# Kernel tuning notes

Measured on AMD Instinct MI355X. Metric: run time of the kernel, lower is better.

Reference implementation:

```python
import jax, jax.numpy as jnp
import numpy as np

B, Q, N, C = 2, 1024, 4096, 768
H, D, REL = 12, 64, 32
SCALE = 1.0 / np.sqrt(D)


def _lin_coords(n_out, n_in):
    # align_corners=True mapping: x_in = x_out * (n_in-1)/(n_out-1)
    pos = jnp.arange(n_out, dtype=jnp.float32) * ((n_in - 1) / (n_out - 1))
    lo = jnp.clip(jnp.floor(pos).astype(jnp.int32), 0, n_in - 1)
    hi = jnp.clip(lo + 1, 0, n_in - 1)
    w = pos - lo.astype(jnp.float32)
    return lo, hi, w


def _interp_bias(bias, q_len, n_len):
    # bias: [H, 32, 32] -> [H, q_len, n_len] bilinear, align_corners=True
    lq, hq, wq = _lin_coords(q_len, REL)
    ln, hn, wn = _lin_coords(n_len, REL)
    b1 = bias[:, lq, :] * (1.0 - wq)[None, :, None] + bias[:, hq, :] * wq[None, :, None]  # [H,q,32]
    b2 = b1[:, :, ln] * (1.0 - wn)[None, None, :] + b1[:, :, hn] * wn[None, None, :]      # [H,q,n]
    return b2


def setup_inputs() -> dict:
    key = jax.random.key(0)
    ks = jax.random.split(key, 11)
    s = 1.0 / np.sqrt(C)
    return {
        "query": jax.random.normal(ks[0], (B, Q, C), jnp.float32),
        "key_value": jax.random.normal(ks[1], (B, N, C), jnp.float32),
        "Wq": jax.random.normal(ks[2], (C, C), jnp.float32) * s,
        "bq": jax.random.normal(ks[3], (C,), jnp.float32) * 0.01,
        "Wk": jax.random.normal(ks[4], (C, C), jnp.float32) * s,
        "bk": jax.random.normal(ks[5], (C,), jnp.float32) * 0.01,
        "Wv": jax.random.normal(ks[6], (C, C), jnp.float32) * s,
        "bv": jax.random.normal(ks[7], (C,), jnp.float32) * 0.01,
        "Wo": jax.random.normal(ks[8], (C, C), jnp.float32) * s,
        "bo": jax.random.normal(ks[9], (C,), jnp.float32) * 0.01,
        "rel_pos_bias": jax.random.normal(ks[10], (H, REL, REL), jnp.float32) * 0.02,
    }


def reference(query, key_value, Wq, bq, Wk, bk, Wv, bv, Wo, bo, rel_pos_bias):
    b, n, c = key_value.shape
    q_len = query.shape[1]
    # projections (dropout in eval mode -> identity)
    q = (query @ Wq + bq).reshape(b, q_len, H, D).transpose(0, 2, 1, 3)      # [B,H,Q,D]
    k = (key_value @ Wk + bk).reshape(b, n, H, D).transpose(0, 2, 1, 3)      # [B,H,N,D]
    v = (key_value @ Wv + bv).reshape(b, n, H, D).transpose(0, 2, 1, 3)      # [B,H,N,D]
    attn = jnp.einsum('bhqd,bhnd->bhqn', q, k) * SCALE
    attn = attn + _interp_bias(rel_pos_bias, q_len, n)[None]                 # [B,H,Q,N]
    p = jax.nn.softmax(attn, axis=-1)
    out = jnp.einsum('bhqn,bhnd->bhqd', p, v)
    out = out.transpose(0, 2, 1, 3).reshape(b, q_len, c)
    return out @ Wo + bo
```

## Files before the change

### kernel.cpp

```cpp
#include <hip/hip_runtime.h>
#include <stdint.h>

typedef unsigned short ushort_t;
typedef __bf16 bf16x8 __attribute__((ext_vector_type(8)));
typedef __bf16 bf16x4v __attribute__((ext_vector_type(4)));
typedef float f32x4 __attribute__((ext_vector_type(4)));
typedef unsigned short us4 __attribute__((ext_vector_type(4)));

#define LOG2E 1.4426950408889634f
#define NEG8L (-11.541560327111707f)
#define QSCALE 0.18033688011110974f

__device__ __forceinline__ ushort_t f2b(float f) {
    unsigned u = __float_as_uint(f);
    unsigned r = (u + 0x7fffu + ((u >> 16) & 1u)) >> 16;
    return (ushort_t)r;
}
__device__ __forceinline__ void gld16(const void* g, void* l) {
    __builtin_amdgcn_global_load_lds(
        (__attribute__((address_space(1))) void*)g,
        (__attribute__((address_space(3))) void*)l,
        16, 0, 0);
}

__global__ __launch_bounds__(256) void prep(
        const float* __restrict__ query, const float* __restrict__ keyv,
        const float* __restrict__ Wq, const float* __restrict__ Wk,
        const float* __restrict__ Wv, const float* __restrict__ Wo,
        const float* __restrict__ rel,
        ushort_t* __restrict__ qc, ushort_t* __restrict__ kvc,
        ushort_t* __restrict__ wtq, ushort_t* __restrict__ wtk,
        ushort_t* __restrict__ wtv, ushort_t* __restrict__ wto,
        ushort_t* __restrict__ b1b, ushort_t* __restrict__ wtab) {
    __shared__ ushort_t tsh[32][33];
    const int bid = blockIdx.x, tid = threadIdx.x;
    if (bid < 7680) {
        const float* src = (bid < 1536) ? query : keyv;
        ushort_t* dst = (bid < 1536) ? qc : kvc;
        int i = ((bid < 1536) ? bid : bid - 1536) * 256 + tid;
        float4 x = ((const float4*)src)[i];
        us4 v; v.x = f2b(x.x); v.y = f2b(x.y); v.z = f2b(x.z); v.w = f2b(x.w);
        ((us4*)dst)[i] = v;
    } else if (bid < 9984) {
        int t = bid - 7680, w = t / 576, tt = t - w * 576;
        const float* in = (w == 0) ? Wq : (w == 1) ? Wk : (w == 2) ? Wv : Wo;
        ushort_t* out = (w == 0) ? wtq : (w == 1) ? wtk : (w == 2) ? wtv : wto;
        int x = tid & 31, y = tid >> 5;
        int bx = (tt % 24) * 32, by = (tt / 24) * 32;
#pragma unroll
        for (int j = 0; j < 32; j += 8)
            tsh[y + j][x] = f2b(in[(size_t)(by + y + j) * 768 + bx + x]);
        __syncthreads();
#pragma unroll
        for (int j = 0; j < 32; j += 8)
            out[(size_t)(bx + y + j) * 768 + by + x] = tsh[x][y + j];
    } else if (bid < 11520) {
        int idx = (bid - 9984) * 256 + tid;
        int j = idx & 31, q = (idx >> 5) & 1023, h = idx >> 15;
        float pos = q * (31.0f / 1023.0f);
        float fl = floorf(pos);
        int lo = (int)fl; if (lo > 31) lo = 31;
        float w = pos - fl;
        int hi = lo + 1; if (hi > 31) hi = 31;
        float vlo = rel[(h * 32 + lo) * 32 + j];
        float vhi = rel[(h * 32 + hi) * 32 + j];
        b1b[idx] = f2b((vlo + (vhi - vlo) * w) * LOG2E);
    } else {
        int n = (bid - 11520) * 256 + tid;
        float pos = n * (31.0f / 4095.0f);
        float fl = floorf(pos);
        int ln = (int)fl; if (ln > 31) ln = 31;
        float wn = pos - fl;
        int hn = ln + 1; if (hn > 31) hn = 31;
        float vals[32];
#pragma unroll
        for (int j = 0; j < 32; ++j) vals[j] = 0.f;
        vals[ln] += 1.0f - wn;
        vals[hn] += wn;
#pragma unroll
        for (int j = 0; j < 32; ++j) wtab[n * 32 + j] = f2b(vals[j]);
    }
}

__device__ __forceinline__ void gemm_store(const float* __restrict__ bias,
                                           f32x4 a, void* out,
                                           int mode, int lsh, float scale,
                                           int mbase, int n) {
    if (mode == 2) {
        int h = n >> 6, d = n & 63;
        int b = mbase >> lsh, l = mbase & ((1 << lsh) - 1);
        float bvf = bias[n];
        us4 v;
        v.x = f2b((a[0] + bvf) * scale);
        v.y = f2b((a[1] + bvf) * scale);
        v.z = f2b((a[2] + bvf) * scale);
        v.w = f2b((a[3] + bvf) * scale);
        *(us4*)((ushort_t*)out + ((size_t)((b * 12 + h) * 64 + d) << lsh) + l) = v;
    } else if (mode == 3) {
        int h = mbase >> 6, dbase = mbase & 63;
        int b = n >> lsh, l = n & ((1 << lsh) - 1);
        us4 v;
        v.x = f2b((a[0] + bias[mbase + 0]) * scale);
        v.y = f2b((a[1] + bias[mbase + 1]) * scale);
        v.z = f2b((a[2] + bias[mbase + 2]) * scale);
        v.w = f2b((a[3] + bias[mbase + 3]) * scale);
        *(us4*)((ushort_t*)out + ((((size_t)(b * 12 + h) << lsh) + l) << 6) + dbase) = v;
    } else {
        float4 v;
        v.x = (a[0] + bias[mbase + 0]) * scale;
        v.y = (a[1] + bias[mbase + 1]) * scale;
        v.z = (a[2] + bias[mbase + 2]) * scale;
        v.w = (a[3] + bias[mbase + 3]) * scale;
        *(float4*)((float*)out + (size_t)n * 768 + mbase) = v;
    }
}

__device__ __forceinline__ void gemm_body128(const ushort_t* __restrict__ A,
                                             const ushort_t* __restrict__ Bt,
                                             const float* __restrict__ bias,
                                             void* __restrict__ out,
                                             int mode, int lsh, float scale,
                                             int m0, int n0,
                                             ushort_t* As, ushort_t* Bs, int tid) {
    const int wave = tid >> 6, lane = tid & 63;
    const int quad = lane >> 4, l15 = lane & 15;
    const int wm = wave >> 1, wn = wave & 1;
    const f32x4 z4 = {0.f, 0.f, 0.f, 0.f};
    f32x4 acc[4][4];
#pragma unroll
    for (int i = 0; i < 4; ++i)
#pragma unroll
        for (int j = 0; j < 4; ++j) acc[i][j] = z4;

    const int arow4 = lane >> 4;
    const int ablk16 = lane & 15;

    for (int kk = 0; kk < 768; kk += 128) {
        __syncthreads();
#pragma unroll
        for (int i = 0; i < 8; ++i) {
            int c = wave * 8 + i;
            int row = c * 4 + arow4;
            int swz = (ablk16 ^ (row & 15)) * 8;
            gld16(A + (size_t)(m0 + row) * 768 + kk + swz, (void*)(As + c * 512));
            gld16(Bt + (size_t)(n0 + row) * 768 + kk + swz, (void*)(Bs + c * 512));
        }
        __syncthreads();
#pragma unroll
        for (int ks = 0; ks < 4; ++ks) {
            bf16x8 af[4], bf[4];
#pragma unroll
            for (int mb = 0; mb < 4; ++mb) {
                int r = wm * 64 + mb * 16 + l15;
                af[mb] = *(const bf16x8*)(As + r * 128 + (((ks * 4 + quad) ^ (r & 15)) * 8));
            }
#pragma unroll
            for (int nb = 0; nb < 4; ++nb) {
                int r = wn * 64 + nb * 16 + l15;
                bf[nb] = *(const bf16x8*)(Bs + r * 128 + (((ks * 4 + quad) ^ (r & 15)) * 8));
            }
#pragma unroll
            for (int mb = 0; mb < 4; ++mb)
#pragma unroll
                for (int nb = 0; nb < 4; ++nb)
                    acc[mb][nb] = __builtin_amdgcn_mfma_f32_16x16x32_bf16(af[mb], bf[nb], acc[mb][nb], 0, 0, 0);
        }
    }

#pragma unroll
    for (int mb = 0; mb < 4; ++mb) {
        int mbase = m0 + wm * 64 + mb * 16 + quad * 4;
#pragma unroll
        for (int nb = 0; nb < 4; ++nb) {
            int n = n0 + wn * 64 + nb * 16 + l15;
            gemm_store(bias, acc[mb][nb], out, mode, lsh, scale, mbase, n);
        }
    }
}

__device__ __forceinline__ void gemm_body64(const ushort_t* __restrict__ A,
                                            const ushort_t* __restrict__ Bt,
                                            const float* __restrict__ bias,
                                            void* __restrict__ out,
                                            int mode, int lsh, float scale,
                                            int m0, int n0,
                                            ushort_t* As, ushort_t* Bs, int tid) {
    const int wave = tid >> 6, lane = tid & 63;
    const int quad = lane >> 4, l15 = lane & 15;
    const f32x4 z4 = {0.f, 0.f, 0.f, 0.f};
    f32x4 acc[4];
#pragma unroll
    for (int j = 0; j < 4; ++j) acc[j] = z4;

    const int arow = lane >> 3;
    const int ablk = lane & 7;
    const int kswz = (ablk ^ arow) * 8;

    for (int kk = 0; kk < 768; kk += 64) {
        __syncthreads();
#pragma unroll
        for (int i = 0; i < 2; ++i) {
            int c = wave * 2 + i;
            gld16(A + (size_t)(m0 + c * 8 + arow) * 768 + kk + kswz, (void*)(As + c * 512));
            gld16(Bt + (size_t)(n0 + c * 8 + arow) * 768 + kk + kswz, (void*)(Bs + c * 512));
        }
        __syncthreads();
#pragma unroll
        for (int ks = 0; ks < 2; ++ks) {
            bf16x8 af, bf[4];
            {
                int r = wave * 16 + l15;
                af = *(const bf16x8*)(As + r * 64 + (((ks * 4 + quad) ^ (r & 7)) * 8));
            }
#pragma unroll
            for (int nb = 0; nb < 4; ++nb) {
                int r = nb * 16 + l15;
                bf[nb] = *(const bf16x8*)(Bs + r * 64 + (((ks * 4 + quad) ^ (r & 7)) * 8));
            }
#pragma unroll
            for (int nb = 0; nb < 4; ++nb)
                acc[nb] = __builtin_amdgcn_mfma_f32_16x16x32_bf16(af, bf[nb], acc[nb], 0, 0, 0);
        }
    }

    int mbase = m0 + wave * 16 + quad * 4;
#pragma unroll
    for (int nb = 0; nb < 4; ++nb) {
        int n = n0 + nb * 16 + l15;
        gemm_store(bias, acc[nb], out, mode, lsh, scale, mbase, n);
    }
}

__global__ __launch_bounds__(256) void proj3(const ushort_t* __restrict__ qc,
                                             const ushort_t* __restrict__ kvc,
                                             const ushort_t* __restrict__ wtq,
                                             const ushort_t* __restrict__ wtk,
                                             const ushort_t* __restrict__ wtv,
                                             const float* __restrict__ bq,
                                             const float* __restrict__ bk,
                                             const float* __restrict__ bv,
                                             ushort_t* __restrict__ qp,
                                             ushort_t* __restrict__ kp,
                                             ushort_t* __restrict__ vtp) {
    __shared__ __align__(16) ushort_t As[128 * 128];
    __shared__ __align__(16) ushort_t Bs[128 * 128];
    const int bid = blockIdx.x, tid = threadIdx.x;
    if (bid < 96) {
        int t = bid;
        int nt = (t & 7) + 8 * ((t >> 3) & 1), mt = t >> 4;
        gemm_body128(wtq, qc, bq, qp, 3, 10, QSCALE, mt * 128, nt * 128, As, Bs, tid);
    } else if (bid < 480) {
        int t = bid - 96;
        int nt = (t & 7) + 8 * ((t >> 3) & 7), mt = t >> 6;
        gemm_body128(wtk, kvc, bk, kp, 3, 12, 1.0f, mt * 128, nt * 128, As, Bs, tid);
    } else {
        int t = bid - 480, mt = t & 63, nt = t >> 6;
        gemm_body128(kvc, wtv, bv, vtp, 2, 12, 1.0f, mt * 128, nt * 128, As, Bs, tid);
    }
}

__global__ __launch_bounds__(256) void gemm_out(const ushort_t* __restrict__ ab,
                                                const ushort_t* __restrict__ wto,
                                                const float* __restrict__ bo,
                                                float* __restrict__ out) {
    __shared__ __align__(16) ushort_t As[64 * 64];
    __shared__ __align__(16) ushort_t Bs[64 * 64];
    const int bid = blockIdx.x, tid = threadIdx.x;
    int j = bid >> 3;
    int nt = (bid & 7) + 8 * (j & 3), mt = j >> 2;
    gemm_body64(wto, ab, bo, out, 4, 0, 1.0f, mt * 64, nt * 64, As, Bs, tid);
}

__global__ __launch_bounds__(256) void attn64s(const ushort_t* __restrict__ qp,
                                               const ushort_t* __restrict__ kp,
                                               const ushort_t* __restrict__ vt,
                                               const ushort_t* __restrict__ b1b,
                                               const ushort_t* __restrict__ wtab,
                                               float* __restrict__ po,
                                               float* __restrict__ pl) {
    __shared__ __align__(16) ushort_t k_s[128 * 64];
    __shared__ __align__(16) ushort_t v_s[64 * 128];
    __shared__ __align__(16) __bf16 pB[4][16 * 136];

    const int tid = threadIdx.x;
    const int wave = tid >> 6, lane = tid & 63;
    const int quad = lane >> 4, l15 = lane & 15;
    const int bid = blockIdx.x;
    const int xcd = bid & 7;
    const int slot = bid >> 3;
    const int g = xcd + 8 * (slot >> 5);
    const int member = slot & 31;
    const int b = g / 12, h = g - b * 12;
    const int qt = member & 15, sp = member >> 4;
    const int q0 = qt * 64;
    const int bh = g;

    const ushort_t* qg = qp + ((size_t)bh * 1024 + q0) * 64;
    const ushort_t* kg = kp + (size_t)bh * 4096 * 64;
    const ushort_t* vg = vt + (size_t)bh * 64 * 4096;

    const int rowq = wave * 16 + l15;
    bf16x8 aq[2];
#pragma unroll
    for (int ks = 0; ks < 2; ++ks)
        aq[ks] = *(const bf16x8*)(qg + (size_t)rowq * 64 + (ks * 4 + quad) * 8);
    bf16x8 ab1 = *(const bf16x8*)(b1b + ((size_t)(h * 1024 + q0 + rowq)) * 32 + quad * 8);

    const f32x4 mC = {NEG8L, NEG8L, NEG8L, NEG8L};
    const f32x4 z4 = {0.f, 0.f, 0.f, 0.f};
    f32x4 o[4];
    float lsum = 0.f;
#pragma unroll
    for (int d = 0; d < 4; ++d) o[d] = z4;

    const int arow = lane >> 3;
    const int ablk = lane & 7;
    const int arow4 = lane >> 4;
    const int ablk16 = lane & 15;
    const int nbase = sp * 2048;
    __bf16* pw = &pB[wave][0];

    for (int nt = 0; nt < 16; ++nt) {
        const int n0 = nbase + nt * 128;
        __syncthreads();
#pragma unroll
        for (int i = 0; i < 4; ++i) {
            int c = wave * 4 + i;
            int krow = c * 8 + arow;
            gld16(kg + (size_t)(n0 + krow) * 64 + (ablk ^ (krow & 7)) * 8,
                  (void*)(k_s + c * 512));
            int vrow = c * 4 + arow4;
            gld16(vg + (size_t)vrow * 4096 + n0 + (ablk16 ^ (vrow & 15)) * 8,
                  (void*)(v_s + c * 512));
        }
        bf16x8 wf[8];
#pragma unroll
        for (int nb = 0; nb < 8; ++nb)
            wf[nb] = *(const bf16x8*)(wtab + (size_t)(n0 + nb * 16 + l15) * 32 + quad * 8);
        __syncthreads();

        f32x4 s[8];
#pragma unroll
        for (int nb = 0; nb < 8; ++nb) {
            s[nb] = __builtin_amdgcn_mfma_f32_16x16x32_bf16(wf[nb], ab1, mC, 0, 0, 0);
            int rn = nb * 16 + l15;
#pragma unroll
            for (int ks = 0; ks < 2; ++ks) {
                bf16x8 bk = *(const bf16x8*)(k_s + rn * 64 + (((ks * 4 + quad) ^ (rn & 7)) * 8));
                s[nb] = __builtin_amdgcn_mfma_f32_16x16x32_bf16(bk, aq[ks], s[nb], 0, 0, 0);
            }
        }
#pragma unroll
        for (int nb = 0; nb < 8; ++nb) {
            bf16x4v pv;
#pragma unroll
            for (int r = 0; r < 4; ++r) {
                float p = exp2f(s[nb][r]);
                lsum += p;
                pv[r] = (__bf16)p;
            }
            *(bf16x4v*)(pw + l15 * 136 + nb * 16 + quad * 4) = pv;
        }
#pragma unroll
        for (int ks = 0; ks < 4; ++ks) {
            bf16x8 bp = *(const bf16x8*)(pw + l15 * 136 + ks * 32 + quad * 8);
#pragma unroll
            for (int dt = 0; dt < 4; ++dt) {
                int rd = dt * 16 + l15;
                bf16x8 av = *(const bf16x8*)(v_s + rd * 128 + (((ks * 4 + quad) ^ (rd & 15)) * 8));
                o[dt] = __builtin_amdgcn_mfma_f32_16x16x32_bf16(av, bp, o[dt], 0, 0, 0);
            }
        }
    }

    lsum += __shfl_xor(lsum, 16, 64);
    lsum += __shfl_xor(lsum, 32, 64);

    const size_t pbase = ((size_t)(sp * 24 + bh)) * 1024;
    const int qrow = q0 + wave * 16 + l15;
    if (lane < 16) pl[pbase + qrow] = lsum;
#pragma unroll
    for (int dt = 0; dt < 4; ++dt)
        *(float4*)(po + (pbase + qrow) * 64 + dt * 16 + quad * 4) = (float4){o[dt][0], o[dt][1], o[dt][2], o[dt][3]};
}

__global__ __launch_bounds__(256) void combine(const float* __restrict__ po,
                                               const float* __restrict__ pl,
                                               ushort_t* __restrict__ ab) {
    int idx = blockIdx.x * 256 + threadIdx.x;
    int e = idx * 4;
    int b = e / 786432;
    int rem = e - b * 786432;
    int q = rem / 768;
    int col = rem - q * 768;
    int h = col >> 6, d = col & 63;
    int bh = b * 12 + h;
    float4 acc = {0.f, 0.f, 0.f, 0.f};
    float l = 0.f;
#pragma unroll
    for (int s = 0; s < 2; ++s) {
        size_t base = ((size_t)(s * 24 + bh)) * 1024 + q;
        float4 v = *(const float4*)(po + base * 64 + d);
        acc.x += v.x; acc.y += v.y; acc.z += v.z; acc.w += v.w;
        l += pl[base];
    }
    float inv = 1.0f / l;
    us4 v;
    v.x = f2b(acc.x * inv); v.y = f2b(acc.y * inv);
    v.z = f2b(acc.z * inv); v.w = f2b(acc.w * inv);
    *(us4*)(ab + (size_t)(b * 1024 + q) * 768 + col) = v;
}

extern "C" void kernel_launch(void* const* d_in, const int* in_sizes, int n_in,
                              void* d_out, int out_size, void* d_ws, size_t ws_size,
                              hipStream_t stream) {
    const float* query = (const float*)d_in[0];
    const float* keyv  = (const float*)d_in[1];
    const float* Wq = (const float*)d_in[2];
    const float* bq = (const float*)d_in[3];
    const float* Wk = (const float*)d_in[4];
    const float* bk = (const float*)d_in[5];
    const float* Wv = (const float*)d_in[6];
    const float* bv = (const float*)d_in[7];
    const float* Wo = (const float*)d_in[8];
    const float* bo = (const float*)d_in[9];
    const float* rel = (const float*)d_in[10];

    char* ws = (char*)d_ws;
    ushort_t* qc   = (ushort_t*)(ws + 0);
    ushort_t* kvc  = (ushort_t*)(ws + 3145728);
    ushort_t* wtq  = (ushort_t*)(ws + 15728640);
    ushort_t* wtk  = (ushort_t*)(ws + 16908288);
    ushort_t* wtv  = (ushort_t*)(ws + 18087936);
    ushort_t* wto  = (ushort_t*)(ws + 19267584);
    ushort_t* qp   = (ushort_t*)(ws + 20447232);
    ushort_t* kp   = (ushort_t*)(ws + 23592960);
    ushort_t* vtp  = (ushort_t*)(ws + 36175872);
    ushort_t* b1b  = (ushort_t*)(ws + 48758784);
    ushort_t* wtab = (ushort_t*)(ws + 49545216);
    ushort_t* ab   = (ushort_t*)(ws + 49807360);
    float*    po   = (float*)(ws + 52953088);
    float*    pl   = (float*)(ws + 65536000);

    prep<<<11536, 256, 0, stream>>>(query, keyv, Wq, Wk, Wv, Wo, rel,
                                    qc, kvc, wtq, wtk, wtv, wto, b1b, wtab);
    proj3<<<864, 256, 0, stream>>>(qc, kvc, wtq, wtk, wtv, bq, bk, bv, qp, kp, vtp);
    attn64s<<<768, 256, 0, stream>>>(qp, kp, vtp, b1b, wtab, po, pl);
    combine<<<1536, 256, 0, stream>>>(po, pl, ab);
    gemm_out<<<384, 256, 0, stream>>>(ab, wto, bo, (float*)d_out);
}
```

Baseline: 204.4 us.

## Use packed bf16 converts, raw exp2, MFMA row sums, and wider K tile

```diff
diff --git a/kernel.cpp b/kernel.cpp
--- a/kernel.cpp
+++ b/kernel.cpp
@@ -3,7 +3,6 @@
 
 typedef unsigned short ushort_t;
 typedef __bf16 bf16x8 __attribute__((ext_vector_type(8)));
-typedef __bf16 bf16x4v __attribute__((ext_vector_type(4)));
 typedef float f32x4 __attribute__((ext_vector_type(4)));
 typedef unsigned short us4 __attribute__((ext_vector_type(4)));
 
@@ -15,6 +14,29 @@
     unsigned u = __float_as_uint(f);
     unsigned r = (u + 0x7fffu + ((u >> 16) & 1u)) >> 16;
     return (ushort_t)r;
+}
+__device__ __forceinline__ unsigned pk2(float a, float b) {
+#if __has_builtin(__builtin_amdgcn_cvt_pk_bf16_f32)
+    auto v = __builtin_amdgcn_cvt_pk_bf16_f32(a, b);
+    return __builtin_bit_cast(unsigned, v);
+#else
+    unsigned ua = __float_as_uint(a), ub = __float_as_uint(b);
+    unsigned ra = (ua + 0x7fffu + ((ua >> 16) & 1u)) >> 16;
+    unsigned rb = (ub + 0x7fffu + ((ub >> 16) & 1u)) >> 16;
+    return ra | (rb << 16);
+#endif
+}
+__device__ __forceinline__ us4 pk4(float a, float b, float c, float d) {
+    union { unsigned u[2]; us4 v; } x;
+    x.u[0] = pk2(a, b); x.u[1] = pk2(c, d);
+    return x.v;
+}
+__device__ __forceinline__ float fexp2(float x) {
+#if __has_builtin(__builtin_amdgcn_exp2f)
+    return __builtin_amdgcn_exp2f(x);
+#else
+    return exp2f(x);
+#endif
 }
 __device__ __forceinline__ void gld16(const void* g, void* l) {
     __builtin_amdgcn_global_load_lds(
@@ -39,8 +61,7 @@
         ushort_t* dst = (bid < 1536) ? qc : kvc;
         int i = ((bid < 1536) ? bid : bid - 1536) * 256 + tid;
         float4 x = ((const float4*)src)[i];
-        us4 v; v.x = f2b(x.x); v.y = f2b(x.y); v.z = f2b(x.z); v.w = f2b(x.w);
-        ((us4*)dst)[i] = v;
+        ((us4*)dst)[i] = pk4(x.x, x.y, x.z, x.w);
     } else if (bid < 9984) {
         int t = bid - 7680, w = t / 576, tt = t - w * 576;
         const float* in = (w == 0) ? Wq : (w == 1) ? Wk : (w == 2) ? Wv : Wo;
@@ -90,21 +111,15 @@
         int h = n >> 6, d = n & 63;
         int b = mbase >> lsh, l = mbase & ((1 << lsh) - 1);
         float bvf = bias[n];
-        us4 v;
-        v.x = f2b((a[0] + bvf) * scale);
-        v.y = f2b((a[1] + bvf) * scale);
-        v.z = f2b((a[2] + bvf) * scale);
-        v.w = f2b((a[3] + bvf) * scale);
-        *(us4*)((ushort_t*)out + ((size_t)((b * 12 + h) * 64 + d) << lsh) + l) = v;
+        *(us4*)((ushort_t*)out + ((size_t)((b * 12 + h) * 64 + d) << lsh) + l) =
+            pk4((a[0] + bvf) * scale, (a[1] + bvf) * scale,
+                (a[2] + bvf) * scale, (a[3] + bvf) * scale);
     } else if (mode == 3) {
         int h = mbase >> 6, dbase = mbase & 63;
         int b = n >> lsh, l = n & ((1 << lsh) - 1);
-        us4 v;
-        v.x = f2b((a[0] + bias[mbase + 0]) * scale);
-        v.y = f2b((a[1] + bias[mbase + 1]) * scale);
-        v.z = f2b((a[2] + bias[mbase + 2]) * scale);
-        v.w = f2b((a[3] + bias[mbase + 3]) * scale);
-        *(us4*)((ushort_t*)out + ((((size_t)(b * 12 + h) << lsh) + l) << 6) + dbase) = v;
+        *(us4*)((ushort_t*)out + ((((size_t)(b * 12 + h) << lsh) + l) << 6) + dbase) =
+            pk4((a[0] + bias[mbase + 0]) * scale, (a[1] + bias[mbase + 1]) * scale,
+                (a[2] + bias[mbase + 2]) * scale, (a[3] + bias[mbase + 3]) * scale);
     } else {
         float4 v;
         v.x = (a[0] + bias[mbase + 0]) * scale;
@@ -192,30 +207,31 @@
 #pragma unroll
     for (int j = 0; j < 4; ++j) acc[j] = z4;
 
-    const int arow = lane >> 3;
-    const int ablk = lane & 7;
-    const int kswz = (ablk ^ arow) * 8;
-
-    for (int kk = 0; kk < 768; kk += 64) {
-        __syncthreads();
-#pragma unroll
-        for (int i = 0; i < 2; ++i) {
-            int c = wave * 2 + i;
-            gld16(A + (size_t)(m0 + c * 8 + arow) * 768 + kk + kswz, (void*)(As + c * 512));
-            gld16(Bt + (size_t)(n0 + c * 8 + arow) * 768 + kk + kswz, (void*)(Bs + c * 512));
-        }
-        __syncthreads();
-#pragma unroll
-        for (int ks = 0; ks < 2; ++ks) {
+    const int arow4 = lane >> 4;
+    const int ablk16 = lane & 15;
+
+    for (int kk = 0; kk < 768; kk += 128) {
+        __syncthreads();
+#pragma unroll
+        for (int i = 0; i < 4; ++i) {
+            int c = wave * 4 + i;
+            int row = c * 4 + arow4;
+            int swz = (ablk16 ^ (row & 15)) * 8;
+            gld16(A + (size_t)(m0 + row) * 768 + kk + swz, (void*)(As + c * 512));
+            gld16(Bt + (size_t)(n0 + row) * 768 + kk + swz, (void*)(Bs + c * 512));
+        }
+        __syncthreads();
+#pragma unroll
+        for (int ks = 0; ks < 4; ++ks) {
             bf16x8 af, bf[4];
             {
                 int r = wave * 16 + l15;
-                af = *(const bf16x8*)(As + r * 64 + (((ks * 4 + quad) ^ (r & 7)) * 8));
+                af = *(const bf16x8*)(As + r * 128 + (((ks * 4 + quad) ^ (r & 15)) * 8));
             }
 #pragma unroll
             for (int nb = 0; nb < 4; ++nb) {
                 int r = nb * 16 + l15;
-                bf[nb] = *(const bf16x8*)(Bs + r * 64 + (((ks * 4 + quad) ^ (r & 7)) * 8));
+                bf[nb] = *(const bf16x8*)(Bs + r * 128 + (((ks * 4 + quad) ^ (r & 15)) * 8));
             }
 #pragma unroll
             for (int nb = 0; nb < 4; ++nb)
@@ -263,8 +279,8 @@
                                                 const ushort_t* __restrict__ wto,
                                                 const float* __restrict__ bo,
                                                 float* __restrict__ out) {
-    __shared__ __align__(16) ushort_t As[64 * 64];
-    __shared__ __align__(16) ushort_t Bs[64 * 64];
+    __shared__ __align__(16) ushort_t As[64 * 128];
+    __shared__ __align__(16) ushort_t Bs[64 * 128];
     const int bid = blockIdx.x, tid = threadIdx.x;
     int j = bid >> 3;
     int nt = (bid & 7) + 8 * (j & 3), mt = j >> 2;
@@ -280,7 +296,7 @@
                                                float* __restrict__ pl) {
     __shared__ __align__(16) ushort_t k_s[128 * 64];
     __shared__ __align__(16) ushort_t v_s[64 * 128];
-    __shared__ __align__(16) __bf16 pB[4][16 * 136];
+    __shared__ __align__(16) ushort_t pB[4][16 * 136];
 
     const int tid = threadIdx.x;
     const int wave = tid >> 6, lane = tid & 63;
@@ -306,10 +322,18 @@
         aq[ks] = *(const bf16x8*)(qg + (size_t)rowq * 64 + (ks * 4 + quad) * 8);
     bf16x8 ab1 = *(const bf16x8*)(b1b + ((size_t)(h * 1024 + q0 + rowq)) * 32 + quad * 8);
 
+    bf16x8 onesv;
+    {
+        union { ushort_t u[8]; bf16x8 v; } c;
+#pragma unroll
+        for (int j = 0; j < 8; ++j) c.u[j] = 0x3F80;
+        onesv = c.v;
+    }
+
     const f32x4 mC = {NEG8L, NEG8L, NEG8L, NEG8L};
     const f32x4 z4 = {0.f, 0.f, 0.f, 0.f};
     f32x4 o[4];
-    float lsum = 0.f;
+    f32x4 ls = z4;
 #pragma unroll
     for (int d = 0; d < 4; ++d) o[d] = z4;
 
@@ -318,7 +342,7 @@
     const int arow4 = lane >> 4;
     const int ablk16 = lane & 15;
     const int nbase = sp * 2048;
-    __bf16* pw = &pB[wave][0];
+    ushort_t* pw = &pB[wave][0];
 
     for (int nt = 0; nt < 16; ++nt) {
         const int n0 = nbase + nt * 128;
@@ -352,18 +376,13 @@
         }
 #pragma unroll
         for (int nb = 0; nb < 8; ++nb) {
-            bf16x4v pv;
-#pragma unroll
-            for (int r = 0; r < 4; ++r) {
-                float p = exp2f(s[nb][r]);
-                lsum += p;
-                pv[r] = (__bf16)p;
-            }
-            *(bf16x4v*)(pw + l15 * 136 + nb * 16 + quad * 4) = pv;
+            *(us4*)(pw + l15 * 136 + nb * 16 + quad * 4) =
+                pk4(fexp2(s[nb][0]), fexp2(s[nb][1]), fexp2(s[nb][2]), fexp2(s[nb][3]));
         }
 #pragma unroll
         for (int ks = 0; ks < 4; ++ks) {
             bf16x8 bp = *(const bf16x8*)(pw + l15 * 136 + ks * 32 + quad * 8);
+            ls = __builtin_amdgcn_mfma_f32_16x16x32_bf16(onesv, bp, ls, 0, 0, 0);
 #pragma unroll
             for (int dt = 0; dt < 4; ++dt) {
                 int rd = dt * 16 + l15;
@@ -373,12 +392,9 @@
         }
     }
 
-    lsum += __shfl_xor(lsum, 16, 64);
-    lsum += __shfl_xor(lsum, 32, 64);
-
     const size_t pbase = ((size_t)(sp * 24 + bh)) * 1024;
     const int qrow = q0 + wave * 16 + l15;
-    if (lane < 16) pl[pbase + qrow] = lsum;
+    if (lane < 16) pl[pbase + qrow] = ls[0];
 #pragma unroll
     for (int dt = 0; dt < 4; ++dt)
         *(float4*)(po + (pbase + qrow) * 64 + dt * 16 + quad * 4) = (float4){o[dt][0], o[dt][1], o[dt][2], o[dt][3]};
@@ -405,10 +421,8 @@
         l += pl[base];
     }
     float inv = 1.0f / l;
-    us4 v;
-    v.x = f2b(acc.x * inv); v.y = f2b(acc.y * inv);
-    v.z = f2b(acc.z * inv); v.w = f2b(acc.w * inv);
-    *(us4*)(ab + (size_t)(b * 1024 + q) * 768 + col) = v;
+    *(us4*)(ab + (size_t)(b * 1024 + q) * 768 + col) =
+        pk4(acc.x * inv, acc.y * inv, acc.z * inv, acc.w * inv);
 }
 
 extern "C" void kernel_launch(void* const* d_in, const int* in_sizes, int n_in,
```

Measured after the change: 203.0 us. About the same (-0.7%).
